# Performance work log

Hardware: AMD Instinct MI355X
Metric: run time of the kernel (lower is better)

Reference implementation:

```python
import jax, jax.numpy as jnp
import numpy as np

PATCH = 3      # patch_size = (3, 3)
STRIDE = 1     # filter_patch_stride == compare_stride == 1
EPS = 1e-12    # F.normalize eps


def extract_patches(x, ph, pw, stride):
    """x: (B, C, H, W) -> (B, nH*nW, C, ph, pw), valid patches."""
    B, C, H, W = x.shape
    oh = (H - ph) // stride + 1
    ow = (W - pw) // stride + 1
    rows = (jnp.arange(oh) * stride)[:, None] + jnp.arange(ph)[None, :]  # (oh, ph)
    cols = (jnp.arange(ow) * stride)[:, None] + jnp.arange(pw)[None, :]  # (ow, pw)
    # gather -> (B, C, oh, ph, ow, pw)
    p = x[:, :, rows[:, :, None, None], cols[None, None, :, :]]
    return p.transpose(0, 2, 4, 1, 3, 5).reshape(B, oh * ow, C, ph, pw)


def l2norm(x, axis):
    # matches F.normalize(p=2): x / max(||x||, eps)
    return x / jnp.maximum(jnp.linalg.norm(x, axis=axis, keepdims=True), EPS)


def setup_inputs() -> dict:
    key = jax.random.key(0)
    k1, k2 = jax.random.split(key)
    pred_style = jax.random.normal(k1, (4, 256, 64, 64), dtype=jnp.float32)
    target_style = jax.random.normal(k2, (4, 256, 64, 64), dtype=jnp.float32)
    return {"pred_style": pred_style, "target_style": target_style}


def reference(pred_style, target_style):
    # patches of the raw (unnormalized) features
    tp = extract_patches(target_style, PATCH, PATCH, STRIDE)   # (B, nP, C, ph, pw)
    pp = extract_patches(pred_style, PATCH, PATCH, STRIDE)     # (B, nP, C, ph, pw)

    # best_match: normalize content feature over channels, style patches over channel dim (dim=2)
    x1n = l2norm(pred_style, axis=1)
    tpn = l2norm(tp, axis=2)
    x1p = extract_patches(x1n, PATCH, PATCH, STRIDE)           # (B, nP, C, ph, pw)

    # conv-as-cosine-correlation == batched patch dot products, then argmax over style patches
    scores = jnp.einsum('bqcij,bpcij->bqp', x1p, tpn)          # (B, nP, nP)
    match = jnp.argmax(scores, axis=2)                         # (B, nP)

    # gather best-matching target patches (indices detached in original via .data)
    new_t = jnp.take_along_axis(tp, match[:, :, None, None, None], axis=1)
    return jnp.mean((pp - new_t) ** 2)
```

## Files before the change

kernel.cpp:

```cpp
#include <hip/hip_runtime.h>
#include <hip/hip_bf16.h>

#define NB 4
#define CH 256
#define HH 64
#define WW 64
#define NPIX 4096
#define OH 62
#define NPATCH 3844
#define KDIM 256
#define EPSN 1e-12f
#define VROW 68
#define SEG 8
#define PST 68

typedef __attribute__((ext_vector_type(8))) short short8;
typedef __attribute__((ext_vector_type(4))) float f32x4;

__device__ __forceinline__ float bf16_to_f32(unsigned short u) {
    return __uint_as_float((unsigned)u << 16);
}
__device__ __forceinline__ unsigned short f32_to_bf16(float f) {
    __hip_bfloat16 h = __float2bfloat16(f);
    return *(unsigned short*)&h;
}

__global__ __launch_bounds__(256) void k_prep(const float* __restrict__ pred,
                                              const float* __restrict__ tgt,
                                              __hip_bfloat16* __restrict__ Xn,
                                              __hip_bfloat16* __restrict__ Tn,
                                              float* __restrict__ ssP, float* __restrict__ invP,
                                              float* __restrict__ ssT, float* __restrict__ invT,
                                              unsigned long long* __restrict__ keys,
                                              float* __restrict__ out) {
    const int bz = blockIdx.y;
    const int b = bz >> 1, which = bz & 1;
    const float* src = (which ? tgt : pred) + (size_t)b * CH * NPIX;
    unsigned short* dst = (unsigned short*)((which ? Tn : Xn) + (size_t)b * NPIX * CH);
    float* ss_g  = (which ? ssT  : ssP)  + b * NPIX;
    float* inv_g = (which ? invT : invP) + b * NPIX;
    const int pix0 = blockIdx.x * 64;
    const int t = threadIdx.x, lane = t & 63, wv = t >> 6;

    int gid = (bz * 64 + blockIdx.x) * 256 + t;
    if (gid < NB * NPATCH) keys[gid] = 0ull;
    if (gid == 0) out[0] = 0.f;

    __shared__ unsigned short stage[CH][PST];
    __shared__ float partial[16][68];
    __shared__ float inv_s[64];

    const int cb = t >> 4, chk = t & 15;
    float ss0 = 0.f, ss1 = 0.f, ss2 = 0.f, ss3 = 0.f;
#pragma unroll
    for (int r = 0; r < 16; ++r) {
        int c = cb * 16 + r;
        float4 v = *(const float4*)&src[(size_t)c * NPIX + pix0 + chk * 4];
        ss0 += v.x * v.x; ss1 += v.y * v.y; ss2 += v.z * v.z; ss3 += v.w * v.w;
        ushort4 sv;
        sv.x = f32_to_bf16(v.x); sv.y = f32_to_bf16(v.y);
        sv.z = f32_to_bf16(v.z); sv.w = f32_to_bf16(v.w);
        *(ushort4*)&stage[c][chk * 4] = sv;
    }
    float4 pv; pv.x = ss0; pv.y = ss1; pv.z = ss2; pv.w = ss3;
    *(float4*)&partial[cb][chk * 4] = pv;
    __syncthreads();
    if (t < 64) {
        float ss = 0.f;
#pragma unroll
        for (int r = 0; r < 16; ++r) ss += partial[r][t];
        float inv = 1.f / fmaxf(sqrtf(ss), EPSN);
        ss_g[pix0 + t] = ss;
        inv_g[pix0 + t] = inv;
        inv_s[t] = inv;
    }
    __syncthreads();
    for (int p = wv; p < 64; p += 4) {
        float iv = inv_s[p];
#pragma unroll
        for (int cc = 0; cc < 4; ++cc) {
            int c = cc * 64 + lane;
            float v = bf16_to_f32(stage[c][p]) * iv;
            dst[(size_t)(pix0 + p) * CH + c] = f32_to_bf16(v);
        }
    }
}

__device__ __forceinline__ void gload_lds16(const void* g, void* l) {
    __builtin_amdgcn_global_load_lds(
        (const __attribute__((address_space(1))) void*)g,
        (__attribute__((address_space(3))) void*)l, 16, 0, 0);
}

__global__ __launch_bounds__(512, 2) void k_gemm(const __hip_bfloat16* __restrict__ A,
                                                 const __hip_bfloat16* __restrict__ Bm,
                                                 unsigned short* __restrict__ Dout) {
    __shared__ __align__(16) short smem[65536];
#define ASOFF(buf) ((buf) * 16384)
#define BSOFF(buf) (32768 + (buf) * 16384)

    const int t = threadIdx.x;
    const int lane = t & 63, wv = t >> 6;
    const int wm = wv >> 2, wn = wv & 3;

    const int bid = ((blockIdx.z << 4) + blockIdx.y) * 16 + blockIdx.x;
    const int swz = ((bid & 7) << 7) + (bid >> 3);
    const int z = swz >> 8, by = (swz >> 4) & 15, bx = swz & 15;

    const int row0 = by * 256, col0 = bx * 256;
    const short* Ag = (const short*)A + (size_t)z * NPIX * CH;
    const short* Bg = (const short*)Bm + (size_t)z * NPIX * CH;
    unsigned short* D = Dout + (size_t)z * NPIX * NPIX;

    const int srow = t >> 3;
    const int kce  = ((t & 7) ^ (srow & 7)) * 8;

    f32x4 acc[8][4] = {};

#define STAGE_K(buf, k0)                                                                   \
    do {                                                                                   \
        _Pragma("unroll")                                                                  \
        for (int rr_ = 0; rr_ < 4; ++rr_)                                                  \
            gload_lds16(Ag + (size_t)(row0 + rr_ * 64 + srow) * KDIM + (k0) + kce,         \
                        &smem[ASOFF(buf) + rr_ * 4096 + wv * 512]);                        \
        _Pragma("unroll")                                                                  \
        for (int rr_ = 0; rr_ < 4; ++rr_)                                                  \
            gload_lds16(Bg + (size_t)(col0 + rr_ * 64 + srow) * KDIM + (k0) + kce,         \
                        &smem[BSOFF(buf) + rr_ * 4096 + wv * 512]);                        \
    } while (0)

    const int rsel = lane & 15, kq = lane >> 4;
    const int rx = rsel & 7;

#define CONSUME(buf)                                                                       \
    do {                                                                                   \
        _Pragma("unroll")                                                                  \
        for (int s = 0; s < 2; ++s) {                                                      \
            const int pk = (((s << 2) + kq) ^ rx) * 8;                                     \
            short8 a_[8], b_[4];                                                           \
            _Pragma("unroll")                                                              \
            for (int mi = 0; mi < 8; ++mi)                                                 \
                a_[mi] = *(const short8*)&smem[ASOFF(buf) + (wm * 128 + mi * 16 + rsel) * 64 + pk]; \
            _Pragma("unroll")                                                              \
            for (int ni = 0; ni < 4; ++ni)                                                 \
                b_[ni] = *(const short8*)&smem[BSOFF(buf) + (wn * 64 + ni * 16 + rsel) * 64 + pk];  \
            _Pragma("unroll")                                                              \
            for (int mi = 0; mi < 8; ++mi)                                                 \
                _Pragma("unroll")                                                          \
                for (int ni = 0; ni < 4; ++ni)                                             \
                    acc[mi][ni] = __builtin_amdgcn_mfma_f32_16x16x32_bf16(b_[ni], a_[mi],  \
                                                                          acc[mi][ni], 0, 0, 0); \
        }                                                                                  \
    } while (0)

#define WAIT_VM(N)                                                  \
    do {                                                            \
        asm volatile("s_waitcnt vmcnt(" #N ")" ::: "memory");       \
        __builtin_amdgcn_sched_barrier(0);                          \
        __builtin_amdgcn_s_barrier();                               \
        __builtin_amdgcn_sched_barrier(0);                          \
    } while (0)

#define WAIT_LGKM_BAR()                                             \
    do {                                                            \
        asm volatile("s_waitcnt lgkmcnt(0)" ::: "memory");          \
        __builtin_amdgcn_sched_barrier(0);                          \
        __builtin_amdgcn_s_barrier();                               \
        __builtin_amdgcn_sched_barrier(0);                          \
    } while (0)

    STAGE_K(0, 0);
    STAGE_K(1, 64);

    WAIT_VM(8);
    CONSUME(0);
    WAIT_LGKM_BAR();
    STAGE_K(0, 128);

    WAIT_VM(8);
    CONSUME(1);
    WAIT_LGKM_BAR();
    STAGE_K(1, 192);

    WAIT_VM(8);
    CONSUME(0);

    WAIT_VM(0);
    CONSUME(1);
#undef WAIT_LGKM_BAR
#undef WAIT_VM
#undef CONSUME
#undef STAGE_K

    const int r16 = lane & 15, c4 = (lane >> 4) * 4;
#pragma unroll
    for (int mi = 0; mi < 8; ++mi) {
        const size_t rowoff = (size_t)(row0 + wm * 128 + mi * 16 + r16) * NPIX;
#pragma unroll
        for (int ni = 0; ni < 4; ++ni) {
            uint2 u;
            u.x = (unsigned)f32_to_bf16(acc[mi][ni][0]) |
                  ((unsigned)f32_to_bf16(acc[mi][ni][1]) << 16);
            u.y = (unsigned)f32_to_bf16(acc[mi][ni][2]) |
                  ((unsigned)f32_to_bf16(acc[mi][ni][3]) << 16);
            *(uint2*)&D[rowoff + col0 + wn * 64 + ni * 16 + c4] = u;
        }
    }
#undef ASOFF
#undef BSOFF
}

__device__ __forceinline__ void load_tile16(const unsigned short* __restrict__ D,
                                            int row, int col, float* f) {
    const unsigned short* rp = D + (size_t)row * NPIX + col;
    uint4 u0 = *(const uint4*)rp;
    uint4 u1 = *(const uint4*)(rp + 8);
    const unsigned* w0 = (const unsigned*)&u0;
    const unsigned* w1 = (const unsigned*)&u1;
#pragma unroll
    for (int w = 0; w < 4; ++w) {
        f[2 * w]         = bf16_to_f32((unsigned short)w0[w]);
        f[2 * w + 1]     = bf16_to_f32((unsigned short)(w0[w] >> 16));
        f[8 + 2 * w]     = bf16_to_f32((unsigned short)w1[w]);
        f[8 + 2 * w + 1] = bf16_to_f32((unsigned short)(w1[w] >> 16));
    }
}

__global__ __launch_bounds__(256) void k_score(const unsigned short* __restrict__ Dbase,
                                               unsigned long long* __restrict__ keys) {
    const int z = blockIdx.z;
    const unsigned short* D = Dbase + (size_t)z * NPIX * NPIX;
    const int t = threadIdx.x;

    const int d = (int)blockIdx.x - 61;
    const int adg = d < 0 ? -d : d;
    const int len = 62 - adg;
    const int s0 = blockIdx.y * SEG;
    if (s0 >= len) return;
    const int steps = min(SEG, len - s0);
    const int qr0 = (d > 0 ? d : 0) + s0;
    const int pr0 = qr0 - d;

    __shared__ __align__(16) float V[64 * VROW];

    const int a = t >> 2, b0 = (t & 3) * 16;
    const int g = t >> 6, qc = t & 63;
    const int qcr = qc < OH ? qc : (OH - 1);
    const int pc0 = g * 16;
    const int kmax = (g == 3) ? 14 : 16;

    float A[16], B[16], C[16];
    load_tile16(D, (qr0 + 0) * 64 + a, (pr0 + 0) * 64 + b0, A);
    load_tile16(D, (qr0 + 1) * 64 + a, (pr0 + 1) * 64 + b0, B);

    for (int k = 0; k < steps; ++k) {
        load_tile16(D, (qr0 + k + 2) * 64 + a, (pr0 + k + 2) * 64 + b0, C);
        float v[16];
#pragma unroll
        for (int e = 0; e < 16; ++e) v[e] = A[e] + B[e] + C[e];
        if (k) __syncthreads();
#pragma unroll
        for (int e = 0; e < 16; e += 4)
            *(f32x4*)&V[a * VROW + b0 + e] = *(const f32x4*)&v[e];
        __syncthreads();

        float r0[16], r1[20], r2[20];
#pragma unroll
        for (int e = 0; e < 16; e += 4)
            *(f32x4*)&r0[e] = *(const f32x4*)&V[qcr * VROW + pc0 + e];
#pragma unroll
        for (int e = 0; e < 20; e += 4)
            *(f32x4*)&r1[e] = *(const f32x4*)&V[(qcr + 1) * VROW + pc0 + e];
#pragma unroll
        for (int e = 0; e < 20; e += 4)
            *(f32x4*)&r2[e] = *(const f32x4*)&V[(qcr + 2) * VROW + pc0 + e];
        float best = -1e30f; int bpc = 0;
#pragma unroll
        for (int kk = 0; kk < 16; ++kk) {
            float s = r0[kk] + r1[kk + 1] + r2[kk + 2];
            if (kk < kmax && s > best) { best = s; bpc = pc0 + kk; }
        }
        if (qc < OH) {
            unsigned u = __float_as_uint(best);
            u = (best >= 0.f) ? (u | 0x80000000u) : ~u;
            unsigned long long key = ((unsigned long long)u << 12)
                                   | (unsigned)((63 - (pr0 + k)) << 6)
                                   | (unsigned)(63 - bpc);
            atomicMax(&keys[(size_t)z * NPATCH + (qr0 + k) * OH + qc], key);
        }
#pragma unroll
        for (int e = 0; e < 16; ++e) { A[e] = B[e]; B[e] = C[e]; }
    }
}

__global__ void k_loss(const unsigned short* __restrict__ Dbase,
                       const unsigned long long* __restrict__ keys,
                       const float* __restrict__ ssPb, const float* __restrict__ invPb,
                       const float* __restrict__ ssTb, const float* __restrict__ invTb,
                       float* __restrict__ out) {
    const int z = blockIdx.y;
    const unsigned short* D = Dbase + (size_t)z * NPIX * NPIX;
    const float* ssP  = ssPb  + z * NPIX;
    const float* invP = invPb + z * NPIX;
    const float* ssT  = ssTb  + z * NPIX;
    const float* invT = invTb + z * NPIX;
    int q = blockIdx.x * 256 + threadIdx.x;
    float acc = 0.f;
    if (q < NPATCH) {
        int qr = q / OH, qc = q - qr * OH;
        int qpix = qr * WW + qc;
        unsigned long long key = keys[(size_t)z * NPATCH + q];
        int mpr = 63 - (int)((key >> 6) & 63);
        int mpc = 63 - (int)(key & 63);
        int mpix = mpr * WW + mpc;
#pragma unroll
        for (int i = 0; i < 3; ++i)
#pragma unroll
            for (int j = 0; j < 3; ++j) {
                int off = i * WW + j;
                int y = qpix + off, x = mpix + off;
                float Dv = bf16_to_f32(D[(size_t)y * NPIX + x]);
                float nP = ssP[y] * invP[y];
                float nT = ssT[x] * invT[x];
                acc += ssP[y] + ssT[x] - 2.f * Dv * nP * nT;
            }
    }
#pragma unroll
    for (int s = 32; s > 0; s >>= 1) acc += __shfl_down(acc, s, 64);
    if ((threadIdx.x & 63) == 0)
        atomicAdd(out, acc * (1.f / 35426304.f));
}

extern "C" void kernel_launch(void* const* d_in, const int* in_sizes, int n_in,
                              void* d_out, int out_size, void* d_ws, size_t ws_size,
                              hipStream_t stream) {
    const float* pred = (const float*)d_in[0];
    const float* tgt  = (const float*)d_in[1];
    char* ws = (char*)d_ws;
    unsigned short*     Dws  = (unsigned short*)(ws);
    __hip_bfloat16*     Xn   = (__hip_bfloat16*)(ws + 134217728);
    __hip_bfloat16*     Tn   = (__hip_bfloat16*)(ws + 142606336);
    float*              ssP  = (float*)(ws + 150994944);
    float*              invP = (float*)(ws + 151060480);
    float*              ssT  = (float*)(ws + 151126016);
    float*              invT = (float*)(ws + 151191552);
    unsigned long long* keys = (unsigned long long*)(ws + 151257088);

    k_prep<<<dim3(64, 8), 256, 0, stream>>>(pred, tgt, Xn, Tn, ssP, invP, ssT, invT,
                                            keys, (float*)d_out);
    k_gemm<<<dim3(16, 16, 4), 512, 0, stream>>>(Xn, Tn, Dws);
    k_score<<<dim3(123, 8, 4), 256, 0, stream>>>(Dws, keys);
    k_loss<<<dim3(16, 4), 256, 0, stream>>>(Dws, keys, ssP, invP, ssT, invT,
                                            (float*)d_out);
}
```

Before: 186.5 us.

## Shrink GEMM tiles, deepen K pipeline, split launches, use DPP in score

```diff
diff --git a/kernel.cpp b/kernel.cpp
--- a/kernel.cpp
+++ b/kernel.cpp
@@ -92,110 +92,96 @@
         (__attribute__((address_space(3))) void*)l, 16, 0, 0);
 }
 
-__global__ __launch_bounds__(512, 2) void k_gemm(const __hip_bfloat16* __restrict__ A,
+__global__ __launch_bounds__(256, 2) void k_gemm(const __hip_bfloat16* __restrict__ A,
                                                  const __hip_bfloat16* __restrict__ Bm,
-                                                 unsigned short* __restrict__ Dout) {
-    __shared__ __align__(16) short smem[65536];
-#define ASOFF(buf) ((buf) * 16384)
-#define BSOFF(buf) (32768 + (buf) * 16384)
+                                                 unsigned short* __restrict__ Dout,
+                                                 int zbase) {
+    __shared__ __align__(16) short smem[24576];
+#define ASOFF(buf) ((buf) * 4096)
+#define BSOFF(buf) (8192 + (buf) * 8192)
 
     const int t = threadIdx.x;
     const int lane = t & 63, wv = t >> 6;
-    const int wm = wv >> 2, wn = wv & 3;
-
-    const int bid = ((blockIdx.z << 4) + blockIdx.y) * 16 + blockIdx.x;
+    const int wn = wv;
+
+    const int bid = ((blockIdx.z << 5) + blockIdx.y) * 16 + blockIdx.x;
     const int swz = ((bid & 7) << 7) + (bid >> 3);
-    const int z = swz >> 8, by = (swz >> 4) & 15, bx = swz & 15;
-
-    const int row0 = by * 256, col0 = bx * 256;
+    const int z = zbase + (swz >> 9), by = (swz >> 4) & 31, bx = swz & 15;
+
+    const int row0 = by * 128, col0 = bx * 256;
     const short* Ag = (const short*)A + (size_t)z * NPIX * CH;
     const short* Bg = (const short*)Bm + (size_t)z * NPIX * CH;
     unsigned short* D = Dout + (size_t)z * NPIX * NPIX;
 
-    const int srow = t >> 3;
-    const int kce  = ((t & 7) ^ (srow & 7)) * 8;
+    const int srow = t >> 2;
+    const int kce  = ((t & 3) ^ (srow & 3)) * 8;
 
     f32x4 acc[8][4] = {};
 
 #define STAGE_K(buf, k0)                                                                   \
     do {                                                                                   \
         _Pragma("unroll")                                                                  \
-        for (int rr_ = 0; rr_ < 4; ++rr_)                                                  \
+        for (int rr_ = 0; rr_ < 2; ++rr_)                                                  \
             gload_lds16(Ag + (size_t)(row0 + rr_ * 64 + srow) * KDIM + (k0) + kce,         \
-                        &smem[ASOFF(buf) + rr_ * 4096 + wv * 512]);                        \
-        _Pragma("unroll")                                                                  \
-        for (int rr_ = 0; rr_ < 4; ++rr_)                                                  \
-            gload_lds16(Bg + (size_t)(col0 + rr_ * 64 + srow) * KDIM + (k0) + kce,         \
-                        &smem[BSOFF(buf) + rr_ * 4096 + wv * 512]);                        \
+                        &smem[ASOFF(buf) + rr_ * 2048 + wv * 512]);                        \
+        _Pragma("unroll")                                                                  \
+        for (int cc_ = 0; cc_ < 4; ++cc_)                                                  \
+            gload_lds16(Bg + (size_t)(col0 + cc_ * 64 + srow) * KDIM + (k0) + kce,         \
+                        &smem[BSOFF(buf) + cc_ * 2048 + wv * 512]);                        \
     } while (0)
 
     const int rsel = lane & 15, kq = lane >> 4;
-    const int rx = rsel & 7;
+    const int pk = (kq ^ (rsel & 3)) * 8;
 
 #define CONSUME(buf)                                                                       \
     do {                                                                                   \
-        _Pragma("unroll")                                                                  \
-        for (int s = 0; s < 2; ++s) {                                                      \
-            const int pk = (((s << 2) + kq) ^ rx) * 8;                                     \
-            short8 a_[8], b_[4];                                                           \
-            _Pragma("unroll")                                                              \
-            for (int mi = 0; mi < 8; ++mi)                                                 \
-                a_[mi] = *(const short8*)&smem[ASOFF(buf) + (wm * 128 + mi * 16 + rsel) * 64 + pk]; \
+        short8 a_[8], b_[4];                                                               \
+        _Pragma("unroll")                                                                  \
+        for (int mi = 0; mi < 8; ++mi)                                                     \
+            a_[mi] = *(const short8*)&smem[ASOFF(buf) + (mi * 16 + rsel) * 32 + pk];       \
+        _Pragma("unroll")                                                                  \
+        for (int ni = 0; ni < 4; ++ni)                                                     \
+            b_[ni] = *(const short8*)&smem[BSOFF(buf) + (wn * 64 + ni * 16 + rsel) * 32 + pk]; \
+        _Pragma("unroll")                                                                  \
+        for (int mi = 0; mi < 8; ++mi)                                                     \
             _Pragma("unroll")                                                              \
             for (int ni = 0; ni < 4; ++ni)                                                 \
-                b_[ni] = *(const short8*)&smem[BSOFF(buf) + (wn * 64 + ni * 16 + rsel) * 64 + pk];  \
-            _Pragma("unroll")                                                              \
-            for (int mi = 0; mi < 8; ++mi)                                                 \
-                _Pragma("unroll")                                                          \
-                for (int ni = 0; ni < 4; ++ni)                                             \
-                    acc[mi][ni] = __builtin_amdgcn_mfma_f32_16x16x32_bf16(b_[ni], a_[mi],  \
-                                                                          acc[mi][ni], 0, 0, 0); \
-        }                                                                                  \
+                acc[mi][ni] = __builtin_amdgcn_mfma_f32_16x16x32_bf16(b_[ni], a_[mi],      \
+                                                                      acc[mi][ni], 0, 0, 0); \
     } while (0)
 
-#define WAIT_VM(N)                                                  \
+#define KITER(it, VMC)                                              \
     do {                                                            \
-        asm volatile("s_waitcnt vmcnt(" #N ")" ::: "memory");       \
+        asm volatile("s_waitcnt vmcnt(" #VMC ")" ::: "memory");     \
         __builtin_amdgcn_sched_barrier(0);                          \
         __builtin_amdgcn_s_barrier();                               \
         __builtin_amdgcn_sched_barrier(0);                          \
-    } while (0)
-
-#define WAIT_LGKM_BAR()                                             \
-    do {                                                            \
+        CONSUME((it) & 1);                                          \
         asm volatile("s_waitcnt lgkmcnt(0)" ::: "memory");          \
         __builtin_amdgcn_sched_barrier(0);                          \
         __builtin_amdgcn_s_barrier();                               \
         __builtin_amdgcn_sched_barrier(0);                          \
+        if ((it) < 6) STAGE_K((it) & 1, ((it) + 2) * 32);           \
     } while (0)
 
     STAGE_K(0, 0);
-    STAGE_K(1, 64);
-
-    WAIT_VM(8);
-    CONSUME(0);
-    WAIT_LGKM_BAR();
-    STAGE_K(0, 128);
-
-    WAIT_VM(8);
-    CONSUME(1);
-    WAIT_LGKM_BAR();
-    STAGE_K(1, 192);
-
-    WAIT_VM(8);
-    CONSUME(0);
-
-    WAIT_VM(0);
-    CONSUME(1);
-#undef WAIT_LGKM_BAR
-#undef WAIT_VM
+    STAGE_K(1, 32);
+    KITER(0, 6);
+    KITER(1, 6);
+    KITER(2, 6);
+    KITER(3, 6);
+    KITER(4, 6);
+    KITER(5, 6);
+    KITER(6, 6);
+    KITER(7, 0);
+#undef KITER
 #undef CONSUME
 #undef STAGE_K
 
     const int r16 = lane & 15, c4 = (lane >> 4) * 4;
 #pragma unroll
     for (int mi = 0; mi < 8; ++mi) {
-        const size_t rowoff = (size_t)(row0 + wm * 128 + mi * 16 + r16) * NPIX;
+        const size_t rowoff = (size_t)(row0 + mi * 16 + r16) * NPIX;
 #pragma unroll
         for (int ni = 0; ni < 4; ++ni) {
             uint2 u;
@@ -245,7 +231,7 @@
 
     const int a = t >> 2, b0 = (t & 3) * 16;
     const int g = t >> 6, qc = t & 63;
-    const int qcr = qc < OH ? qc : (OH - 1);
+    const int l15 = qc & 15;
     const int pc0 = g * 16;
     const int kmax = (g == 3) ? 14 : 16;
 
@@ -264,20 +250,34 @@
             *(f32x4*)&V[a * VROW + b0 + e] = *(const f32x4*)&v[e];
         __syncthreads();
 
-        float r0[16], r1[20], r2[20];
-#pragma unroll
-        for (int e = 0; e < 16; e += 4)
-            *(f32x4*)&r0[e] = *(const f32x4*)&V[qcr * VROW + pc0 + e];
+        float r[20];
 #pragma unroll
         for (int e = 0; e < 20; e += 4)
-            *(f32x4*)&r1[e] = *(const f32x4*)&V[(qcr + 1) * VROW + pc0 + e];
-#pragma unroll
-        for (int e = 0; e < 20; e += 4)
-            *(f32x4*)&r2[e] = *(const f32x4*)&V[(qcr + 2) * VROW + pc0 + e];
+            *(f32x4*)&r[e] = *(const f32x4*)&V[qc * VROW + pc0 + e];
+        float rB[20], rC[20];
+        if (l15 >= 14) {
+            int rowC = qc + 2 > 63 ? 63 : qc + 2;
+#pragma unroll
+            for (int e = 0; e < 20; e += 4)
+                *(f32x4*)&rC[e] = *(const f32x4*)&V[rowC * VROW + pc0 + e];
+            if (l15 == 15) {
+                int rowB = qc + 1 > 63 ? 63 : qc + 1;
+#pragma unroll
+                for (int e = 0; e < 20; e += 4)
+                    *(f32x4*)&rB[e] = *(const f32x4*)&V[rowB * VROW + pc0 + e];
+            }
+        }
+
         float best = -1e30f; int bpc = 0;
 #pragma unroll
         for (int kk = 0; kk < 16; ++kk) {
-            float s = r0[kk] + r1[kk + 1] + r2[kk + 2];
+            float v1 = __uint_as_float((unsigned)__builtin_amdgcn_mov_dpp(
+                           (int)__float_as_uint(r[kk + 1]), 0x101, 0xf, 0xf, true));
+            float v2 = __uint_as_float((unsigned)__builtin_amdgcn_mov_dpp(
+                           (int)__float_as_uint(r[kk + 2]), 0x102, 0xf, 0xf, true));
+            if (l15 == 15) v1 = rB[kk + 1];
+            if (l15 >= 14) v2 = rC[kk + 2];
+            float s = r[kk] + v1 + v2;
             if (kk < kmax && s > best) { best = s; bpc = pc0 + kk; }
         }
         if (qc < OH) {
@@ -348,7 +348,8 @@
 
     k_prep<<<dim3(64, 8), 256, 0, stream>>>(pred, tgt, Xn, Tn, ssP, invP, ssT, invT,
                                             keys, (float*)d_out);
-    k_gemm<<<dim3(16, 16, 4), 512, 0, stream>>>(Xn, Tn, Dws);
+    k_gemm<<<dim3(16, 32, 2), 256, 0, stream>>>(Xn, Tn, Dws, 0);
+    k_gemm<<<dim3(16, 32, 2), 256, 0, stream>>>(Xn, Tn, Dws, 2);
     k_score<<<dim3(123, 8, 4), 256, 0, stream>>>(Dws, keys);
     k_loss<<<dim3(16, 4), 256, 0, stream>>>(Dws, keys, ssP, invP, ssT, invT,
                                             (float*)d_out);
```

New measurement: 198.7 us. +6.5%, slower.
